# Optimization experiments

Hardware: AMD Instinct MI355X
Metric: run time of the kernel (lower is better)

Reference implementation:

```python
import jax, jax.numpy as jnp
import numpy as np

N_HEADS = 16
CHUNK = 128  # chunk size for blocked causal linear attention


def _phi(x):
    # feature map: elu(x) + 1 (strictly positive)
    return jax.nn.elu(x) + 1.0


def setup_inputs() -> dict:
    key = jax.random.key(0)
    ks = jax.random.split(key, 5)
    d = 1024
    scale = (2.0 / (d + d)) ** 0.5  # xavier_uniform-like std
    W = lambda k: jax.random.normal(k, (d, d), jnp.float32) * scale
    return {
        "x": jax.random.normal(ks[0], (4, 4096, d), jnp.float32),
        "Wq": W(ks[1]), "bq": jnp.zeros((d,), jnp.float32),
        "Wk": W(ks[2]), "bk": jnp.zeros((d,), jnp.float32),
        "Wv": W(ks[3]), "bv": jnp.zeros((d,), jnp.float32),
        "Wo": W(ks[4]), "bo": jnp.zeros((d,), jnp.float32),
    }


def reference(x, Wq, bq, Wk, bk, Wv, bv, Wo, bo):
    b, s, dm = x.shape
    h = N_HEADS
    d = dm // h

    def proj(W, bias):
        # (b, s, dm) -> (b*h, s, d)
        y = x @ W.T + bias
        return y.reshape(b, s, h, d).transpose(0, 2, 1, 3).reshape(b * h, s, d)

    q = _phi(proj(Wq, bq))
    k = _phi(proj(Wk, bk))
    v = proj(Wv, bv)

    C = CHUNK
    n = s // C
    # (b*h, s, d) -> (n_chunks, b*h, C, d) for scan over chunks
    to_chunks = lambda t: t.reshape(b * h, n, C, d).transpose(1, 0, 2, 3)
    qc, kc, vc = to_chunks(q), to_chunks(k), to_chunks(v)
    mask = jnp.tril(jnp.ones((C, C), bool))  # causal within chunk

    def step(carry, inp):
        S, z = carry  # S: (bh, d, d) running sum of k v^T; z: (bh, d) running sum of k
        qi, ki, vi = inp  # each (bh, C, d)
        scores = jnp.einsum('bqd,bkd->bqk', qi, ki)
        scores = jnp.where(mask, scores, jnp.zeros((), scores.dtype))
        num = jnp.einsum('bqk,bkd->bqd', scores, vi) + jnp.einsum('bqd,bde->bqe', qi, S)
        kcum = jnp.cumsum(ki, axis=1) + z[:, None, :]
        den = jnp.sum(qi * kcum, axis=-1, keepdims=True)
        out = num / den
        S2 = S + jnp.einsum('bkd,bke->bde', ki, vi)
        z2 = z + ki.sum(axis=1)
        return (S2, z2), out

    init = (jnp.zeros((b * h, d, d), x.dtype), jnp.zeros((b * h, d), x.dtype))
    _, outs = jax.lax.scan(step, init, (qc, kc, vc))  # outs: (n, bh, C, d)
    out = outs.transpose(1, 0, 2, 3).reshape(b, h, s, d).transpose(0, 2, 1, 3).reshape(b, s, dm)
    return out @ Wo.T + bo
```

## Files before the change

kernel.cpp:

```cpp
#include <hip/hip_runtime.h>
#include <hip/hip_bf16.h>

typedef __attribute__((ext_vector_type(8))) short bf16x8;
typedef __attribute__((ext_vector_type(4))) short bf16x4;
typedef __attribute__((ext_vector_type(4))) float floatx4;
typedef unsigned short u16;
typedef unsigned int u32;

#define DM 1024
#define SEQ 4096
#define NH 16
#define HD 64
#define CHUNK 128

__device__ __forceinline__ float bf2f(u16 x) {
    u32 u = ((u32)x) << 16;
    return __builtin_bit_cast(float, u);
}
__device__ __forceinline__ u16 f2bf(float f) {
    u32 u = __builtin_bit_cast(u32, f);
    u32 r = u + 0x7FFF + ((u >> 16) & 1);
    return (u16)(r >> 16);
}
__device__ __forceinline__ bf16x8 cvt8(const float* p) {
    floatx4 a = *(const floatx4*)p;
    floatx4 b = *(const floatx4*)(p + 4);
    bf16x8 r;
    r[0] = (short)f2bf(a[0]); r[1] = (short)f2bf(a[1]);
    r[2] = (short)f2bf(a[2]); r[3] = (short)f2bf(a[3]);
    r[4] = (short)f2bf(b[0]); r[5] = (short)f2bf(b[1]);
    r[6] = (short)f2bf(b[2]); r[7] = (short)f2bf(b[3]);
    return r;
}
__device__ __forceinline__ void async_copy16(const u16* gsrc, u16* ldst) {
    __builtin_amdgcn_global_load_lds(
        (const __attribute__((address_space(1))) void*)gsrc,
        (__attribute__((address_space(3))) void*)ldst, 16, 0, 0);
}

__global__ void cvt_w_k(const float* __restrict__ Wq, const float* __restrict__ Wk,
                        const float* __restrict__ Wv, const float* __restrict__ Wo,
                        u16* __restrict__ Wqkv, u16* __restrict__ Wob)
{
    int g = blockIdx.x * 256 + threadIdx.x;
    int w = g >> 17;
    int off = g & 131071;
    const float* src = (w == 0) ? Wq : (w == 1) ? Wk : (w == 2) ? Wv : Wo;
    u16* dst = (w < 3) ? (Wqkv + ((size_t)w << 20)) : Wob;
    *(bf16x8*)&dst[(size_t)off * 8] = cvt8(src + (size_t)off * 8);
}

__global__ void cvt_x_k(const float* __restrict__ xs, u16* __restrict__ xb)
{
    size_t g = (size_t)blockIdx.x * 256 + threadIdx.x;
    *(bf16x8*)&xb[g * 8] = cvt8(xs + g * 8);
}

__global__ __launch_bounds__(256, 4) void qkv_gemm_k(
    const u16* __restrict__ xb, const u16* __restrict__ Wqkv,
    const float* __restrict__ bq, const float* __restrict__ bk,
    const float* __restrict__ bv,
    u16* __restrict__ Qh, u16* __restrict__ Kh, u16* __restrict__ Vh,
    int mblocks)
{
    __shared__ __align__(16) u16 sh[2][128 * 64];
    u16* aSh = sh[0];
    u16* bSh = sh[1];
    int t = threadIdx.x, lane = t & 63, w = t >> 6;
    int q = lane >> 4, ln = lane & 15;
    int wm = (w & 1) * 64, wn = (w >> 1) * 64;
    int bid = blockIdx.x;
    int xcd = bid & 7, local = bid >> 3;
    int mPerX = mblocks >> 3;
    int ml = local % mPerX, nn = local / mPerX;
    int m0 = (xcd * mPerX + ml) * 128, n0 = nn * 128;
    int wgr = t & 192;
    floatx4 acc[4][4] = {};

    for (int k0 = 0; k0 < DM; k0 += 64) {
#pragma unroll
        for (int i = 0; i < 4; ++i) {
            int gi = i * 256 + t;
            int r = gi >> 3;
            int c = (gi & 7) ^ (r & 7);
            async_copy16(xb + (size_t)(m0 + r) * DM + k0 + c * 8,
                         aSh + (size_t)(i * 256 + wgr) * 8);
            async_copy16(Wqkv + (size_t)(n0 + r) * DM + k0 + c * 8,
                         bSh + (size_t)(i * 256 + wgr) * 8);
        }
        __builtin_amdgcn_s_waitcnt(0);
        __syncthreads();
#pragma unroll
        for (int ks = 0; ks < 2; ++ks) {
            int cg = ks * 4 + q;
            bf16x8 af[4], bfv[4];
#pragma unroll
            for (int tm = 0; tm < 4; ++tm) {
                int m = wm + tm * 16 + ln;
                af[tm] = *(const bf16x8*)&aSh[(m * 8 + (cg ^ (m & 7))) * 8];
            }
#pragma unroll
            for (int tn = 0; tn < 4; ++tn) {
                int n = wn + tn * 16 + ln;
                bfv[tn] = *(const bf16x8*)&bSh[(n * 8 + (cg ^ (n & 7))) * 8];
            }
#pragma unroll
            for (int tm = 0; tm < 4; ++tm)
#pragma unroll
                for (int tn = 0; tn < 4; ++tn)
                    acc[tm][tn] = __builtin_amdgcn_mfma_f32_16x16x32_bf16(
                        af[tm], bfv[tn], acc[tm][tn], 0, 0, 0);
        }
        __syncthreads();
    }
    int proj = n0 >> 10, colb = n0 & 1023;
    const float* bias = (proj == 0) ? bq : (proj == 1) ? bk : bv;
    u16* plane = (proj == 0) ? Qh : (proj == 1) ? Kh : Vh;
    u16* cSh = sh[0];
#pragma unroll
    for (int tn = 0; tn < 4; ++tn) {
        int lc = wn + tn * 16 + ln;
        float bb = bias[colb + lc];
        int gr = lc >> 3, lo = lc & 7;
#pragma unroll
        for (int tm = 0; tm < 4; ++tm) {
            int lrb = wm + tm * 16 + q * 4;
#pragma unroll
            for (int r = 0; r < 4; ++r) {
                int lr = lrb + r;
                float v = acc[tm][tn][r] + bb;
                if (proj < 2) v = (v > 0.f) ? (v + 1.f) : __expf(v);
                cSh[lr * 128 + ((gr & 8) | ((gr ^ lr) & 7)) * 8 + lo] = f2bf(v);
            }
        }
    }
    __syncthreads();
    int head0 = colb >> 6;
    size_t blk = (size_t)(m0 >> 12);
    int mrow = m0 & 4095;
#pragma unroll
    for (int h = 0; h < 2; ++h) {
        u16* pb = plane + ((blk * NH + head0 + h) * SEQ + mrow) * HD;
#pragma unroll
        for (int it = 0; it < 4; ++it) {
            int gi = it * 256 + t;
            int s = gi >> 3, g = gi & 7;
            *(bf16x8*)&pb[(size_t)gi * 8] =
                *(const bf16x8*)&cSh[s * 128 + ((h * 8) | (g ^ (s & 7))) * 8];
        }
    }
}

__global__ __launch_bounds__(256, 2) void out_gemm_k(
    const u16* __restrict__ Ah, const u16* __restrict__ Wob,
    const float* __restrict__ bo, float* __restrict__ out, int mblocks)
{
    __shared__ __align__(16) u16 lds[32768];
    int t = threadIdx.x, lane = t & 63, w = t >> 6;
    int q = lane >> 4, ln = lane & 15;
    int wm = (w & 1) * 64, wn = (w >> 1) * 64;
    int bid = blockIdx.x;
    int xcd = bid & 7, local = bid >> 3;
    int mPerX = mblocks >> 3;
    int ml = local % mPerX, nn = local / mPerX;
    int m0 = (xcd * mPerX + ml) * 128, n0 = nn * 128;
    int wgr = t & 192;
    floatx4 acc[4][4] = {};

    auto STAGE = [&](int kk, int buf) {
        int k0 = kk * 64;
        u16* aS = lds + buf * 16384;
        u16* bS = aS + 8192;
#pragma unroll
        for (int i = 0; i < 4; ++i) {
            int gi = i * 256 + t;
            int r = gi >> 3;
            int c = (gi & 7) ^ (r & 7);
            int rr = m0 + r;
            async_copy16(Ah + (((size_t)((rr >> 12) * NH + (k0 >> 6))) << 18)
                            + (size_t)((rr & 4095) << 6) + (size_t)(c * 8),
                         aS + (size_t)(i * 256 + wgr) * 8);
            async_copy16(Wob + (size_t)(n0 + r) * DM + k0 + c * 8,
                         bS + (size_t)(i * 256 + wgr) * 8);
        }
    };

    STAGE(0, 0);
    __syncthreads();
    for (int tt = 0; tt < 16; ++tt) {
        int p = tt & 1;
        if (tt < 15) STAGE(tt + 1, p ^ 1);
        const u16* aS = lds + p * 16384;
        const u16* bS = aS + 8192;
#pragma unroll
        for (int ks = 0; ks < 2; ++ks) {
            int cg = ks * 4 + q;
            bf16x8 af[4], bfv[4];
#pragma unroll
            for (int tm = 0; tm < 4; ++tm) {
                int m = wm + tm * 16 + ln;
                af[tm] = *(const bf16x8*)&aS[(m * 8 + (cg ^ (m & 7))) * 8];
            }
#pragma unroll
            for (int tn = 0; tn < 4; ++tn) {
                int n = wn + tn * 16 + ln;
                bfv[tn] = *(const bf16x8*)&bS[(n * 8 + (cg ^ (n & 7))) * 8];
            }
#pragma unroll
            for (int tm = 0; tm < 4; ++tm)
#pragma unroll
                for (int tn = 0; tn < 4; ++tn)
                    acc[tm][tn] = __builtin_amdgcn_mfma_f32_16x16x32_bf16(
                        af[tm], bfv[tn], acc[tm][tn], 0, 0, 0);
        }
        __syncthreads();
    }
#pragma unroll
    for (int tn = 0; tn < 4; ++tn) {
        int gn = n0 + wn + tn * 16 + ln;
        float bb = bo[gn];
#pragma unroll
        for (int tm = 0; tm < 4; ++tm) {
            int gmb = m0 + wm + tm * 16 + q * 4;
#pragma unroll
            for (int r = 0; r < 4; ++r)
                out[(size_t)(gmb + r) * DM + gn] = acc[tm][tn][r] + bb;
        }
    }
}

__global__ __launch_bounds__(256, 1) void chunk_stats_k(
    const u16* __restrict__ Kh, const u16* __restrict__ Vh,
    u16* __restrict__ Sc, float* __restrict__ Zc)
{
    __shared__ __align__(16) u16 kSh[128 * 64];
    __shared__ __align__(16) u16 vSh[128 * 64];
    __shared__ float zpart[4][64];
    int t = threadIdx.x;
    int bhc = blockIdx.x;
    const u16* Kb = Kh + ((size_t)(bhc >> 5) * SEQ + (size_t)(bhc & 31) * CHUNK) * HD;
    const u16* Vb = Vh + ((size_t)(bhc >> 5) * SEQ + (size_t)(bhc & 31) * CHUNK) * HD;
#pragma unroll
    for (int i = 0; i < 4; ++i) {
        int g = i * 256 + t;
        *(bf16x8*)&kSh[g * 8] = *(const bf16x8*)&Kb[(size_t)g * 8];
        *(bf16x8*)&vSh[g * 8] = *(const bf16x8*)&Vb[(size_t)g * 8];
    }
    __syncthreads();
    int tD = t & 15, tE = t >> 4;
    float acc[4][4] = {};
#pragma unroll 8
    for (int r = 0; r < 128; ++r) {
        bf16x4 vq = *(const bf16x4*)&vSh[r * 64 + tE * 4];
        bf16x4 kq = *(const bf16x4*)&kSh[r * 64 + tD * 4];
        float vf[4], kf[4];
#pragma unroll
        for (int i = 0; i < 4; ++i) { vf[i] = bf2f((u16)vq[i]); kf[i] = bf2f((u16)kq[i]); }
#pragma unroll
        for (int a = 0; a < 4; ++a)
#pragma unroll
            for (int b = 0; b < 4; ++b) acc[a][b] += vf[a] * kf[b];
    }
    u16* So = Sc + (size_t)bhc * HD * HD;
#pragma unroll
    for (int a = 0; a < 4; ++a) {
        bf16x4 sv;
#pragma unroll
        for (int b = 0; b < 4; ++b) sv[b] = (short)f2bf(acc[a][b]);
        *(bf16x4*)&So[(tE * 4 + a) * HD + tD * 4] = sv;
    }
    {
        int dz = t & 63, qz = t >> 6;
        float z = 0.f;
#pragma unroll
        for (int r = 0; r < 32; ++r) z += bf2f(kSh[(qz * 32 + r) * 64 + dz]);
        zpart[qz][dz] = z;
    }
    __syncthreads();
    if (t < 64)
        Zc[(size_t)bhc * HD + t] =
            zpart[0][t] + zpart[1][t] + zpart[2][t] + zpart[3][t];
}

__global__ void prefix_k(u16* __restrict__ Sc, float* __restrict__ Zc)
{
    int bh = blockIdx.x, y = blockIdx.y, t = threadIdx.x;
    if (y < 32) {
        size_t base = (size_t)bh * 32 * 4096 + y * 128 + t;
        u16 vals[32];
#pragma unroll
        for (int c = 0; c < 32; ++c) vals[c] = Sc[base + (size_t)c * 4096];
        float run = 0.f;
#pragma unroll
        for (int c = 0; c < 32; ++c) {
            float cur = bf2f(vals[c]);
            Sc[base + (size_t)c * 4096] = f2bf(run);
            run += cur;
        }
    } else if (t < 64) {
        size_t base = (size_t)bh * 32 * 64 + t;
        float zv[32];
#pragma unroll
        for (int c = 0; c < 32; ++c) zv[c] = Zc[base + (size_t)c * 64];
        float run = 0.f;
#pragma unroll
        for (int c = 0; c < 32; ++c) {
            Zc[base + (size_t)c * 64] = run;
            run += zv[c];
        }
    }
}

__global__ __launch_bounds__(256, 1) void attn_out_k(
    const u16* Qh, const u16* __restrict__ Kh,
    const u16* __restrict__ Vh, const u16* __restrict__ Sp,
    const float* __restrict__ Zp, u16* Qw)
{
    __shared__ __align__(16) u16 vtSh[64 * 136];
    __shared__ __align__(16) u16 pSh[128 * 136];
    __shared__ float psum[128];
    __shared__ float qzs[128];
    int t = threadIdx.x, lane = t & 63, w = t >> 6;
    int q = lane >> 4, ln = lane & 15;
    int bhc = blockIdx.x, bh = bhc >> 5, ch = bhc & 31;
    const u16* Qb = Qh + ((size_t)bh * SEQ + (size_t)ch * CHUNK) * HD;
    const u16* Kb = Kh + ((size_t)bh * SEQ + (size_t)ch * CHUNK) * HD;
    const u16* Vb = Vh + ((size_t)bh * SEQ + (size_t)ch * CHUNK) * HD;
    const u16* Spb = Sp + (size_t)bhc * HD * HD;
    const float* Zpb = Zp + (size_t)bhc * HD;

#pragma unroll
    for (int i = 0; i < 4; ++i) {
        int g = i * 256 + t;
        int k = g >> 3, e0 = (g & 7) * 8;
        bf16x8 vv = *(const bf16x8*)&Vb[(size_t)k * HD + e0];
#pragma unroll
        for (int j = 0; j < 8; ++j) vtSh[(e0 + j) * 136 + k] = (u16)vv[j];
    }

    int wm = (w & 1) * 64, wn = (w >> 1) * 64;
    bf16x8 afr[2][4];
#pragma unroll
    for (int ks = 0; ks < 2; ++ks)
#pragma unroll
        for (int tm = 0; tm < 4; ++tm) {
            int m = wm + tm * 16 + ln;
            afr[ks][tm] = *(const bf16x8*)&Qb[(size_t)m * HD + ks * 32 + q * 8];
        }
    floatx4 acc[4][4] = {};
#pragma unroll
    for (int ks = 0; ks < 2; ++ks) {
        bf16x8 bfr[4];
#pragma unroll
        for (int tn = 0; tn < 4; ++tn) {
            int n = wn + tn * 16 + ln;
            bfr[tn] = *(const bf16x8*)&Kb[(size_t)n * HD + ks * 32 + q * 8];
        }
#pragma unroll
        for (int tm = 0; tm < 4; ++tm)
#pragma unroll
            for (int tn = 0; tn < 4; ++tn)
                acc[tm][tn] = __builtin_amdgcn_mfma_f32_16x16x32_bf16(
                    afr[ks][tm], bfr[tn], acc[tm][tn], 0, 0, 0);
    }
#pragma unroll
    for (int tm = 0; tm < 4; ++tm) {
        int rb = wm + tm * 16 + q * 4;
#pragma unroll
        for (int tn = 0; tn < 4; ++tn) {
            int cc = wn + tn * 16 + ln;
#pragma unroll
            for (int r = 0; r < 4; ++r) {
                float v = (cc <= rb + r) ? acc[tm][tn][r] : 0.f;
                pSh[(rb + r) * 136 + cc] = f2bf(v);
            }
        }
    }
    __syncthreads();
    if (t < 128) {
        const u16* prow = &pSh[t * 136];
        float s = 0.f;
#pragma unroll
        for (int i = 0; i < 16; ++i) {
            bf16x8 pv = *(const bf16x8*)&prow[i * 8];
#pragma unroll
            for (int j = 0; j < 8; ++j) s += bf2f((u16)pv[j]);
        }
        psum[t] = s;
    } else {
        int row = t - 128;
        float s = 0.f;
#pragma unroll
        for (int i = 0; i < 8; ++i) {
            bf16x8 qv = *(const bf16x8*)&Qb[(size_t)row * HD + i * 8];
#pragma unroll
            for (int j = 0; j < 8; ++j) s += bf2f((u16)qv[j]) * Zpb[i * 8 + j];
        }
        qzs[row] = s;
    }
    __syncthreads();

    int wn2 = (w >> 1) * 32;
    floatx4 acc2[4][2] = {};
#pragma unroll
    for (int ks = 0; ks < 4; ++ks) {
        bf16x8 ap[4], bv[2];
#pragma unroll
        for (int tm = 0; tm < 4; ++tm) {
            int m = wm + tm * 16 + ln;
            ap[tm] = *(const bf16x8*)&pSh[m * 136 + ks * 32 + q * 8];
        }
#pragma unroll
        for (int tn = 0; tn < 2; ++tn) {
            int n = wn2 + tn * 16 + ln;
            bv[tn] = *(const bf16x8*)&vtSh[n * 136 + ks * 32 + q * 8];
        }
#pragma unroll
        for (int tm = 0; tm < 4; ++tm)
#pragma unroll
            for (int tn = 0; tn < 2; ++tn)
                acc2[tm][tn] = __builtin_amdgcn_mfma_f32_16x16x32_bf16(
                    ap[tm], bv[tn], acc2[tm][tn], 0, 0, 0);
    }
#pragma unroll
    for (int ks = 0; ks < 2; ++ks) {
        bf16x8 bs[2];
#pragma unroll
        for (int tn = 0; tn < 2; ++tn) {
            int n = wn2 + tn * 16 + ln;
            bs[tn] = *(const bf16x8*)&Spb[(size_t)n * HD + ks * 32 + q * 8];
        }
#pragma unroll
        for (int tm = 0; tm < 4; ++tm)
#pragma unroll
            for (int tn = 0; tn < 2; ++tn)
                acc2[tm][tn] = __builtin_amdgcn_mfma_f32_16x16x32_bf16(
                    afr[ks][tm], bs[tn], acc2[tm][tn], 0, 0, 0);
    }
    __syncthreads();
#pragma unroll
    for (int tm = 0; tm < 4; ++tm) {
        int rb = wm + tm * 16 + q * 4;
#pragma unroll
        for (int r = 0; r < 4; ++r) {
            int mrow = rb + r;
            float inv = 1.0f / fmaxf(psum[mrow] + qzs[mrow], 1e-20f);
#pragma unroll
            for (int tn = 0; tn < 2; ++tn) {
                int e = wn2 + tn * 16 + ln;
                pSh[mrow * 72 + e] = f2bf(acc2[tm][tn][r] * inv);
            }
        }
    }
    __syncthreads();
    size_t obase = ((size_t)bh * SEQ + (size_t)ch * CHUNK) * HD;
#pragma unroll
    for (int j = 0; j < 4; ++j) {
        int ci = j * 256 + t;
        *(bf16x8*)&Qw[obase + (size_t)ci * 8] =
            *(const bf16x8*)&pSh[(ci >> 3) * 72 + (ci & 7) * 8];
    }
}

extern "C" void kernel_launch(void* const* d_in, const int* in_sizes, int n_in,
                              void* d_out, int out_size, void* d_ws, size_t ws_size,
                              hipStream_t stream) {
    const float* x  = (const float*)d_in[0];
    const float* Wq = (const float*)d_in[1];
    const float* bq = (const float*)d_in[2];
    const float* Wk = (const float*)d_in[3];
    const float* bk = (const float*)d_in[4];
    const float* Wv = (const float*)d_in[5];
    const float* bv = (const float*)d_in[6];
    const float* Wo = (const float*)d_in[7];
    const float* bo = (const float*)d_in[8];
    float* out = (float*)d_out;

    const size_t PLANE = (size_t)NH * SEQ * HD;
    const size_t FIXED = (3 * (size_t)DM * DM + (size_t)DM * DM) * 2;
    const size_t PER_BATCH = 4 * PLANE * 2 + (size_t)NH * 32 * 4096 * 2
                           + (size_t)NH * 32 * HD * 4;
    if (ws_size < FIXED + PER_BATCH) return;
    int nb = (ws_size >= FIXED + 4 * PER_BATCH) ? 4
           : (ws_size >= FIXED + 2 * PER_BATCH) ? 2 : 1;

    char* p0 = (char*)d_ws;
    u16* Wqkv = (u16*)p0;                       p0 += 3 * (size_t)DM * DM * 2;
    u16* Wob  = (u16*)p0;                       p0 += (size_t)DM * DM * 2;

    cvt_w_k<<<dim3(2048), dim3(256), 0, stream>>>(Wq, Wk, Wv, Wo, Wqkv, Wob);

    for (int b0 = 0; b0 < 4; b0 += nb) {
        char* p = p0;
        u16* xb = (u16*)p;  p += (size_t)nb * PLANE * 2;
        u16* Qh = (u16*)p;  p += (size_t)nb * PLANE * 2;
        u16* Kh = (u16*)p;  p += (size_t)nb * PLANE * 2;
        u16* Vh = (u16*)p;  p += (size_t)nb * PLANE * 2;
        u16* Sc = (u16*)p;  p += (size_t)nb * NH * 32 * 4096 * 2;
        float* Zc = (float*)p;
        const float* xs = x + (size_t)b0 * SEQ * DM;
        int mb128 = nb * 32;

        cvt_x_k<<<dim3(nb * 2048), dim3(256), 0, stream>>>(xs, xb);
        qkv_gemm_k<<<dim3(24 * mb128), dim3(256), 0, stream>>>(
            xb, Wqkv, bq, bk, bv, Qh, Kh, Vh, mb128);
        chunk_stats_k<<<dim3(nb * 512), dim3(256), 0, stream>>>(Kh, Vh, Sc, Zc);
        prefix_k<<<dim3(nb * 16, 33), dim3(128), 0, stream>>>(Sc, Zc);
        attn_out_k<<<dim3(nb * 512), dim3(256), 0, stream>>>(Qh, Kh, Vh, Sc, Zc, Qh);
        out_gemm_k<<<dim3(8 * mb128), dim3(256), 0, stream>>>(
            Qh, Wob, bo, out + (size_t)b0 * SEQ * DM, mb128);
    }
}
```

Measured before the change: 380.6 us.

## Store V pre-transposed per chunk and use MFMA for chunk KV stats

The QKV GEMM epilogue now writes V transposed per 128-row chunk ([e][k] layout), so attn_out_k reads V^T fragments directly from global memory instead of building a transposed LDS copy. chunk_stats_k replaces its scalar FMA outer-product loop with MFMA over a transposed K tile in LDS and the pre-transposed V. Launch bounds change: the QKV GEMM drops to 2 blocks per CU and attn_out_k rises to 4, trading register headroom for occupancy. Risks include uncoalesced global fragment loads of V^T in attn_out_k and bank conflicts in the scattered K transpose into LDS.

```diff
diff --git a/kernel.cpp b/kernel.cpp
--- a/kernel.cpp
+++ b/kernel.cpp
@@ -56,7 +56,7 @@
     *(bf16x8*)&xb[g * 8] = cvt8(xs + g * 8);
 }
 
-__global__ __launch_bounds__(256, 4) void qkv_gemm_k(
+__global__ __launch_bounds__(256, 2) void qkv_gemm_k(
     const u16* __restrict__ xb, const u16* __restrict__ Wqkv,
     const float* __restrict__ bq, const float* __restrict__ bk,
     const float* __restrict__ bv,
@@ -115,38 +115,71 @@
     }
     int proj = n0 >> 10, colb = n0 & 1023;
     const float* bias = (proj == 0) ? bq : (proj == 1) ? bk : bv;
-    u16* plane = (proj == 0) ? Qh : (proj == 1) ? Kh : Vh;
     u16* cSh = sh[0];
-#pragma unroll
-    for (int tn = 0; tn < 4; ++tn) {
-        int lc = wn + tn * 16 + ln;
-        float bb = bias[colb + lc];
-        int gr = lc >> 3, lo = lc & 7;
-#pragma unroll
-        for (int tm = 0; tm < 4; ++tm) {
-            int lrb = wm + tm * 16 + q * 4;
-#pragma unroll
-            for (int r = 0; r < 4; ++r) {
-                int lr = lrb + r;
-                float v = acc[tm][tn][r] + bb;
-                if (proj < 2) v = (v > 0.f) ? (v + 1.f) : __expf(v);
-                cSh[lr * 128 + ((gr & 8) | ((gr ^ lr) & 7)) * 8 + lo] = f2bf(v);
-            }
-        }
-    }
-    __syncthreads();
     int head0 = colb >> 6;
     size_t blk = (size_t)(m0 >> 12);
     int mrow = m0 & 4095;
-#pragma unroll
-    for (int h = 0; h < 2; ++h) {
-        u16* pb = plane + ((blk * NH + head0 + h) * SEQ + mrow) * HD;
-#pragma unroll
-        for (int it = 0; it < 4; ++it) {
-            int gi = it * 256 + t;
-            int s = gi >> 3, g = gi & 7;
-            *(bf16x8*)&pb[(size_t)gi * 8] =
-                *(const bf16x8*)&cSh[s * 128 + ((h * 8) | (g ^ (s & 7))) * 8];
+    if (proj < 2) {
+        u16* plane = (proj == 0) ? Qh : Kh;
+#pragma unroll
+        for (int tn = 0; tn < 4; ++tn) {
+            int lc = wn + tn * 16 + ln;
+            float bb = bias[colb + lc];
+            int gr = lc >> 3, lo = lc & 7;
+#pragma unroll
+            for (int tm = 0; tm < 4; ++tm) {
+                int lrb = wm + tm * 16 + q * 4;
+#pragma unroll
+                for (int r = 0; r < 4; ++r) {
+                    int lr = lrb + r;
+                    float v = acc[tm][tn][r] + bb;
+                    v = (v > 0.f) ? (v + 1.f) : __expf(v);
+                    cSh[lr * 128 + ((gr & 8) | ((gr ^ lr) & 7)) * 8 + lo] = f2bf(v);
+                }
+            }
+        }
+        __syncthreads();
+#pragma unroll
+        for (int h = 0; h < 2; ++h) {
+            u16* pb = plane + ((blk * NH + head0 + h) * SEQ + mrow) * HD;
+#pragma unroll
+            for (int it = 0; it < 4; ++it) {
+                int gi = it * 256 + t;
+                int s = gi >> 3, g = gi & 7;
+                *(bf16x8*)&pb[(size_t)gi * 8] =
+                    *(const bf16x8*)&cSh[s * 128 + ((h * 8) | (g ^ (s & 7))) * 8];
+            }
+        }
+    } else {
+        int chk = mrow >> 7;
+#pragma unroll
+        for (int tn = 0; tn < 4; ++tn) {
+            int lc = wn + tn * 16 + ln;
+            float bb = bias[colb + lc];
+#pragma unroll
+            for (int tm = 0; tm < 4; ++tm) {
+                int lrb = wm + tm * 16 + q * 4;
+#pragma unroll
+                for (int r = 0; r < 4; ++r) {
+                    int lr = lrb + r;
+                    float v = acc[tm][tn][r] + bb;
+                    cSh[lc * 128 + (((lr >> 3) ^ (lc & 7)) * 8) + (lr & 7)]
+                        = f2bf(v);
+                }
+            }
+        }
+        __syncthreads();
+#pragma unroll
+        for (int h = 0; h < 2; ++h) {
+            u16* pb = Vh + (((blk * NH + head0 + h) * 32 + chk) << 13);
+#pragma unroll
+            for (int it = 0; it < 4; ++it) {
+                int ci = it * 256 + t;
+                int lc = h * 64 + (ci >> 4);
+                int g = ci & 15;
+                *(bf16x8*)&pb[(size_t)ci * 8] =
+                    *(const bf16x8*)&cSh[lc * 128 + ((g ^ (lc & 7)) * 8)];
+            }
         }
     }
 }
@@ -230,52 +263,64 @@
 }
 
 __global__ __launch_bounds__(256, 1) void chunk_stats_k(
-    const u16* __restrict__ Kh, const u16* __restrict__ Vh,
+    const u16* __restrict__ Kh, const u16* __restrict__ Vt,
     u16* __restrict__ Sc, float* __restrict__ Zc)
 {
-    __shared__ __align__(16) u16 kSh[128 * 64];
-    __shared__ __align__(16) u16 vSh[128 * 64];
+    __shared__ __align__(16) u16 ktSh[64 * 130];
     __shared__ float zpart[4][64];
-    int t = threadIdx.x;
-    int bhc = blockIdx.x;
-    const u16* Kb = Kh + ((size_t)(bhc >> 5) * SEQ + (size_t)(bhc & 31) * CHUNK) * HD;
-    const u16* Vb = Vh + ((size_t)(bhc >> 5) * SEQ + (size_t)(bhc & 31) * CHUNK) * HD;
+    int t = threadIdx.x, lane = t & 63, w = t >> 6;
+    int q = lane >> 4, ln = lane & 15;
+    int bhc = blockIdx.x, bh = bhc >> 5, ch = bhc & 31;
+    const u16* Kb = Kh + ((size_t)bh * SEQ + (size_t)ch * CHUNK) * HD;
+    const u16* Vtb = Vt + ((size_t)bh * 32 + ch) * 8192;
+
 #pragma unroll
     for (int i = 0; i < 4; ++i) {
-        int g = i * 256 + t;
-        *(bf16x8*)&kSh[g * 8] = *(const bf16x8*)&Kb[(size_t)g * 8];
-        *(bf16x8*)&vSh[g * 8] = *(const bf16x8*)&Vb[(size_t)g * 8];
-    }
-    __syncthreads();
-    int tD = t & 15, tE = t >> 4;
-    float acc[4][4] = {};
-#pragma unroll 8
-    for (int r = 0; r < 128; ++r) {
-        bf16x4 vq = *(const bf16x4*)&vSh[r * 64 + tE * 4];
-        bf16x4 kq = *(const bf16x4*)&kSh[r * 64 + tD * 4];
-        float vf[4], kf[4];
-#pragma unroll
-        for (int i = 0; i < 4; ++i) { vf[i] = bf2f((u16)vq[i]); kf[i] = bf2f((u16)kq[i]); }
-#pragma unroll
-        for (int a = 0; a < 4; ++a)
-#pragma unroll
-            for (int b = 0; b < 4; ++b) acc[a][b] += vf[a] * kf[b];
-    }
-    u16* So = Sc + (size_t)bhc * HD * HD;
-#pragma unroll
-    for (int a = 0; a < 4; ++a) {
-        bf16x4 sv;
-#pragma unroll
-        for (int b = 0; b < 4; ++b) sv[b] = (short)f2bf(acc[a][b]);
-        *(bf16x4*)&So[(tE * 4 + a) * HD + tD * 4] = sv;
-    }
+        int gi = i * 256 + t;
+        int r = gi >> 3, d0 = (gi & 7) * 8;
+        bf16x8 kv = *(const bf16x8*)&Kb[(size_t)r * HD + d0];
+#pragma unroll
+        for (int j = 0; j < 8; ++j) ktSh[(d0 + j) * 130 + r] = (u16)kv[j];
+    }
+    __syncthreads();
+
     {
         int dz = t & 63, qz = t >> 6;
         float z = 0.f;
 #pragma unroll
-        for (int r = 0; r < 32; ++r) z += bf2f(kSh[(qz * 32 + r) * 64 + dz]);
+        for (int r = 0; r < 32; ++r) z += bf2f(ktSh[dz * 130 + qz * 32 + r]);
         zpart[qz][dz] = z;
     }
+
+    int we = (w & 1) * 32, wd = (w >> 1) * 32;
+    floatx4 acc[2][2] = {};
+#pragma unroll
+    for (int ks = 0; ks < 4; ++ks) {
+        bf16x8 af[2], bf[2];
+#pragma unroll
+        for (int fm = 0; fm < 2; ++fm)
+            af[fm] = *(const bf16x8*)&Vtb[(size_t)(we + fm * 16 + ln) * 128
+                                          + ks * 32 + q * 8];
+#pragma unroll
+        for (int fn = 0; fn < 2; ++fn)
+            bf[fn] = *(const bf16x8*)&ktSh[(wd + fn * 16 + ln) * 130
+                                           + ks * 32 + q * 8];
+#pragma unroll
+        for (int fm = 0; fm < 2; ++fm)
+#pragma unroll
+            for (int fn = 0; fn < 2; ++fn)
+                acc[fm][fn] = __builtin_amdgcn_mfma_f32_16x16x32_bf16(
+                    af[fm], bf[fn], acc[fm][fn], 0, 0, 0);
+    }
+    u16* So = Sc + (size_t)bhc * HD * HD;
+#pragma unroll
+    for (int fm = 0; fm < 2; ++fm)
+#pragma unroll
+        for (int fn = 0; fn < 2; ++fn)
+#pragma unroll
+            for (int r = 0; r < 4; ++r)
+                So[(we + fm * 16 + q * 4 + r) * HD + wd + fn * 16 + ln]
+                    = f2bf(acc[fm][fn][r]);
     __syncthreads();
     if (t < 64)
         Zc[(size_t)bhc * HD + t] =
@@ -311,12 +356,11 @@
     }
 }
 
-__global__ __launch_bounds__(256, 1) void attn_out_k(
+__global__ __launch_bounds__(256, 4) void attn_out_k(
     const u16* Qh, const u16* __restrict__ Kh,
-    const u16* __restrict__ Vh, const u16* __restrict__ Sp,
+    const u16* __restrict__ Vt, const u16* __restrict__ Sp,
     const float* __restrict__ Zp, u16* Qw)
 {
-    __shared__ __align__(16) u16 vtSh[64 * 136];
     __shared__ __align__(16) u16 pSh[128 * 136];
     __shared__ float psum[128];
     __shared__ float qzs[128];
@@ -325,18 +369,9 @@
     int bhc = blockIdx.x, bh = bhc >> 5, ch = bhc & 31;
     const u16* Qb = Qh + ((size_t)bh * SEQ + (size_t)ch * CHUNK) * HD;
     const u16* Kb = Kh + ((size_t)bh * SEQ + (size_t)ch * CHUNK) * HD;
-    const u16* Vb = Vh + ((size_t)bh * SEQ + (size_t)ch * CHUNK) * HD;
+    const u16* Vtb = Vt + ((size_t)bh * 32 + ch) * 8192;
     const u16* Spb = Sp + (size_t)bhc * HD * HD;
     const float* Zpb = Zp + (size_t)bhc * HD;
-
-#pragma unroll
-    for (int i = 0; i < 4; ++i) {
-        int g = i * 256 + t;
-        int k = g >> 3, e0 = (g & 7) * 8;
-        bf16x8 vv = *(const bf16x8*)&Vb[(size_t)k * HD + e0];
-#pragma unroll
-        for (int j = 0; j < 8; ++j) vtSh[(e0 + j) * 136 + k] = (u16)vv[j];
-    }
 
     int wm = (w & 1) * 64, wn = (w >> 1) * 64;
     bf16x8 afr[2][4];
@@ -413,7 +448,7 @@
 #pragma unroll
         for (int tn = 0; tn < 2; ++tn) {
             int n = wn2 + tn * 16 + ln;
-            bv[tn] = *(const bf16x8*)&vtSh[n * 136 + ks * 32 + q * 8];
+            bv[tn] = *(const bf16x8*)&Vtb[(size_t)n * 128 + ks * 32 + q * 8];
         }
 #pragma unroll
         for (int tm = 0; tm < 4; ++tm)
```

Result: faster. 359.9 us (-5.4%).
